# Kernel optimization log

Hardware: AMD Instinct MI355X
Metric: run time of the kernel (lower is better)

## Reference

```python
import jax, jax.numpy as jnp
import numpy as np

N_NODES = 100000
E_HALF = 2000000  # edges come in two mirrored halves (two classes per node pair)
IN_DIM, HID = 5, 16


def setup_inputs() -> dict:
    key = jax.random.key(0)
    ks = jax.random.split(key, 8)
    x = jax.random.normal(ks[0], (N_NODES, IN_DIM), dtype=jnp.float32)
    e_half = jax.random.randint(ks[1], (2, E_HALF), 0, N_NODES)
    edges = jnp.concatenate([e_half, e_half], axis=1)  # [2, 2*E_HALF]
    edge_attr = jax.random.uniform(ks[2], (2 * E_HALF, 2), dtype=jnp.float32)
    detector_labels = jax.random.bernoulli(ks[3], 0.5, (N_NODES,))
    s = 1.0 / np.sqrt(IN_DIM)
    W_rel = jax.random.uniform(ks[4], (HID, IN_DIM), minval=-s, maxval=s, dtype=jnp.float32)
    b_rel = jax.random.uniform(ks[5], (HID,), minval=-s, maxval=s, dtype=jnp.float32)
    W_root = jax.random.uniform(ks[6], (HID, IN_DIM), minval=-s, maxval=s, dtype=jnp.float32)
    s2 = 1.0 / np.sqrt(2 * HID + 1)
    k7, k8 = jax.random.split(ks[7])
    W_lin = jax.random.uniform(k7, (1, 2 * HID + 1), minval=-s2, maxval=s2, dtype=jnp.float32)
    b_lin = jax.random.uniform(k8, (1,), minval=-s2, maxval=s2, dtype=jnp.float32)
    return {
        "x": x, "edges": edges, "edge_attr": edge_attr,
        "detector_labels": detector_labels,
        "W_rel": W_rel, "b_rel": b_rel, "W_root": W_root,
        "W_lin": W_lin, "b_lin": b_lin,
    }


def reference(x, edges, edge_attr, detector_labels, W_rel, b_rel, W_root, W_lin, b_lin):
    N = x.shape[0]
    src, dst = edges[0], edges[1]
    # GraphConv(aggr='add'): out_i = W_root x_i + W_rel * sum_{(j->i)} w_e * x_j + b_rel
    w = edge_attr[:, 1]
    msg = x[src] * w[:, None]                                  # [E, 5]
    agg = jax.ops.segment_sum(msg, dst, num_segments=N)        # [N, 5]
    h = jnp.tanh(agg @ W_rel.T + b_rel + x @ W_root.T)         # [N, 16]
    # SplitSyndromes: keep edges whose both endpoints are detector nodes
    valid = detector_labels[src] & detector_labels[dst]
    vidx = jnp.nonzero(valid)[0]                               # data-dependent (eager)
    e = edges[:, vidx]
    ea = edge_attr[vidx]
    # gather-concat-linear edge scoring
    feat = jnp.concatenate([h[e[0]], ea[:, :1], h[e[1]]], axis=-1)  # [nv, 33]
    score = feat @ W_lin.T + b_lin                             # [nv, 1]
    nv = score.shape[0]
    half = nv // 2
    score2 = score.reshape(-1, half)                           # [2, half]
    classes2 = ea[:, 1].reshape(-1, half)
    mi = jnp.argmin(score2, axis=0)
    cols = jnp.arange(half)
    return e[:, :half], score2[mi, cols], classes2[mi, cols]
```

## Files before the change

kernel.cpp:

```cpp
#include <hip/hip_runtime.h>
#include <hip/hip_bf16.h>

#define HID 16
#define IN_DIM 5
#define PAD 8

#define FXS 64.0f
#define FXI 0.015625f

__global__ void pack_labels(const int* __restrict__ lab, unsigned long long* __restrict__ bits,
                            int N) {
    int n = blockIdx.x * 256 + threadIdx.x;
    bool p = (n < N) && (lab[n] != 0);
    unsigned long long m = __ballot(p);
    if ((threadIdx.x & 63) == 0) bits[n >> 6] = m;
}

__global__ void scatter_count(const int* __restrict__ src, const int* __restrict__ dst,
                              const unsigned long long* __restrict__ bits,
                              const float2* __restrict__ ea2,
                              const float* __restrict__ x,
                              const float* __restrict__ Wlin,
                              unsigned long long* __restrict__ agg,
                              int* __restrict__ counts,
                              int* __restrict__ stS, int* __restrict__ stD,
                              float* __restrict__ stP, float* __restrict__ stC,
                              int EH) {
    int i = blockIdx.x * 256 + threadIdx.x;
    bool v = false;
    int s = 0, d = 0;
    float scpart = 0.f, cls = 0.f;
    if (i < EH) {
        s = src[i];
        d = dst[i];
        bool ls = (bits[s >> 6] >> (s & 63)) & 1;
        bool ld = (bits[d >> 6] >> (d & 63)) & 1;
        v = ls && ld;
        if (ld || v) {
            float2 eaA = ea2[i];
            float2 eaB = ea2[(size_t)i + EH];
            if (ld) {
                float w = eaA.y + eaB.y;
                const float* xs = x + (size_t)s * IN_DIM;
                unsigned long long a = 0;
#pragma unroll
                for (int k = 0; k < IN_DIM; k++) {
                    int q = __float2int_rn(xs[k] * w * FXS);
                    a += (unsigned long long)(long long)q << (12 * k);
                }
                atomicAdd(&agg[(size_t)d * PAD], a);
            }
            if (v) {
                float w16 = Wlin[HID];
                float p0 = w16 * eaA.x;
                float p1 = w16 * eaB.x;
                if (p1 < p0) { scpart = p1; cls = eaB.y; }
                else         { scpart = p0; cls = eaA.y; }
            }
        }
    }
    unsigned long long m = __ballot(v);
    int lane = threadIdx.x & 63, wid = threadIdx.x >> 6;
    __shared__ int wc[4];
    if (lane == 0) wc[wid] = __popcll(m);
    __syncthreads();
    if (threadIdx.x == 0) counts[blockIdx.x] = wc[0] + wc[1] + wc[2] + wc[3];
    if (!v) return;
    int wexcl = 0;
    for (int k = 0; k < wid; k++) wexcl += wc[k];
    int slot = blockIdx.x * 256 + wexcl + __popcll(m & ((1ull << lane) - 1ull));
    stS[slot] = s;
    stD[slot] = d;
    stP[slot] = scpart;
    stC[slot] = cls;
}

__device__ __forceinline__ float decode_field(unsigned long long& T) {
    int r = (int)(T & 0xFFFull);
    int s = (r >= 2048) ? r - 4096 : r;
    T = (T - (unsigned long long)(long long)s) >> 12;
    return (float)s * FXI;
}

__global__ void compute_uv(const float* __restrict__ x,
                           const unsigned long long* __restrict__ agg,
                           const int* __restrict__ lab,
                           const float* __restrict__ Wrel, const float* __restrict__ brel,
                           const float* __restrict__ Wroot, const float* __restrict__ Wlin,
                           float2* __restrict__ uv, int N) {
    __shared__ float sWrel[HID * IN_DIM];
    __shared__ float sWroot[HID * IN_DIM];
    __shared__ float sBrel[HID];
    __shared__ float sWl[2 * HID + 1];
    int t = threadIdx.x;
    if (t < HID * IN_DIM) sWrel[t] = Wrel[t];
    else if (t < 2 * HID * IN_DIM) sWroot[t - HID * IN_DIM] = Wroot[t - HID * IN_DIM];
    else if (t < 2 * HID * IN_DIM + HID) sBrel[t - 2 * HID * IN_DIM] = brel[t - 2 * HID * IN_DIM];
    else if (t < 2 * HID * IN_DIM + HID + 2 * HID + 1)
        sWl[t - 2 * HID * IN_DIM - HID] = Wlin[t - 2 * HID * IN_DIM - HID];
    __syncthreads();

    int n = blockIdx.x * 256 + threadIdx.x;
    if (n >= N) return;
    if (!lab[n]) return;

    unsigned long long T = agg[(size_t)n * PAD];
    float a[IN_DIM], xv[IN_DIM];
#pragma unroll
    for (int d = 0; d < IN_DIM; d++) a[d] = decode_field(T);
#pragma unroll
    for (int d = 0; d < IN_DIM; d++) xv[d] = x[(size_t)n * IN_DIM + d];

    float u = 0.f, vv = 0.f;
#pragma unroll
    for (int k = 0; k < HID; k++) {
        float acc = sBrel[k];
#pragma unroll
        for (int d = 0; d < IN_DIM; d++)
            acc += a[d] * sWrel[k * IN_DIM + d] + xv[d] * sWroot[k * IN_DIM + d];
        float hk = tanhf(acc);
        u += sWl[k] * hk;
        vv += sWl[HID + 1 + k] * hk;
    }
    uv[n] = make_float2(u, vv);
}

__global__ void scan_counts(const int* __restrict__ counts, int* __restrict__ offs, int nb) {
    __shared__ int waveSums[16];
    int tid = threadIdx.x;
    int base = tid * 8;
    int vals[8];
    int tsum = 0;
#pragma unroll
    for (int k = 0; k < 8; k++) {
        int idx = base + k;
        vals[k] = (idx < nb) ? counts[idx] : 0;
        tsum += vals[k];
    }
    int lane = tid & 63, wid = tid >> 6;
    int scan = tsum;
#pragma unroll
    for (int off = 1; off < 64; off <<= 1) {
        int u = __shfl_up(scan, off, 64);
        if (lane >= off) scan += u;
    }
    if (lane == 63) waveSums[wid] = scan;
    __syncthreads();
    if (wid == 0 && lane < 16) {
        int s = waveSums[lane];
#pragma unroll
        for (int off = 1; off < 16; off <<= 1) {
            int u = __shfl_up(s, off, 64);
            if (lane >= off) s += u;
        }
        waveSums[lane] = s;
    }
    __syncthreads();
    int waveBase = (wid > 0) ? waveSums[wid - 1] : 0;
    int excl = waveBase + scan - tsum;
#pragma unroll
    for (int k = 0; k < 8; k++) {
        int idx = base + k;
        if (idx < nb) offs[idx] = excl;
        excl += vals[k];
    }
}

__global__ void emit_out(const int* __restrict__ stS, const int* __restrict__ stD,
                         const float* __restrict__ stP, const float* __restrict__ stC,
                         const float2* __restrict__ uv, const float* __restrict__ blin,
                         const int* __restrict__ counts, const int* __restrict__ offs,
                         float* __restrict__ out, int K) {
    int b = blockIdx.x;
    int cnt = counts[b];
    int t = threadIdx.x;
    if (t >= cnt) return;
    int slot = b * 256 + t;
    int s = stS[slot];
    int d = stD[slot];
    float sc = blin[0] + uv[s].x + uv[d].y + stP[slot];
    int r = offs[b] + t;
    out[r] = (float)s;
    out[(size_t)K + r] = (float)d;
    out[2 * (size_t)K + r] = sc;
    out[3 * (size_t)K + r] = stC[slot];
}

extern "C" void kernel_launch(void* const* d_in, const int* in_sizes, int n_in,
                              void* d_out, int out_size, void* d_ws, size_t ws_size,
                              hipStream_t stream) {
    const float* x     = (const float*)d_in[0];
    const int*   edges = (const int*)d_in[1];
    const float* ea    = (const float*)d_in[2];
    const int*   lab   = (const int*)d_in[3];
    const float* Wrel  = (const float*)d_in[4];
    const float* brel  = (const float*)d_in[5];
    const float* Wroot = (const float*)d_in[6];
    const float* Wlin  = (const float*)d_in[7];
    const float* blin  = (const float*)d_in[8];

    const int N  = in_sizes[0] / IN_DIM;
    const int E  = in_sizes[1] / 2;
    const int EH = E / 2;
    const int K  = out_size / 4;

    const int* src = edges;
    const int* dst = edges + E;
    const float2* ea2 = (const float2*)ea;
    const int nb = (EH + 255) / 256;
    const int nslots = nb * 256;

    char* ws = (char*)d_ws;
    size_t off = 0;
    unsigned long long* agg = (unsigned long long*)(ws + off); off += (size_t)N * PAD * 8;
    float2* uv = (float2*)(ws + off); off += (size_t)N * 8;
    unsigned long long* bits = (unsigned long long*)(ws + off);
    off += (size_t)(((N + 63) / 64) * 8 + 255) / 256 * 256;
    int* counts = (int*)(ws + off); off += (size_t)(nb * 4 + 255) / 256 * 256;
    int* offs   = (int*)(ws + off); off += (size_t)(nb * 4 + 255) / 256 * 256;
    int*   stS = (int*)(ws + off);   off += (size_t)nslots * 4;
    int*   stD = (int*)(ws + off);   off += (size_t)nslots * 4;
    float* stP = (float*)(ws + off); off += (size_t)nslots * 4;
    float* stC = (float*)(ws + off); off += (size_t)nslots * 4;

    float* out = (float*)d_out;

    hipMemsetAsync(agg, 0, (size_t)N * PAD * 8, stream);
    pack_labels<<<(N + 255) / 256, 256, 0, stream>>>(lab, bits, N);
    scatter_count<<<nb, 256, 0, stream>>>(src, dst, bits, ea2, x, Wlin, agg, counts,
                                          stS, stD, stP, stC, EH);
    compute_uv<<<(N + 255) / 256, 256, 0, stream>>>(x, agg, lab, Wrel, brel, Wroot, Wlin, uv, N);
    scan_counts<<<1, 1024, 0, stream>>>(counts, offs, nb);
    emit_out<<<nb, 256, 0, stream>>>(stS, stD, stP, stC, uv, blin, counts, offs, out, K);
}
```

Measured before the change: 181.1 us.

## Process four edges per thread with vector loads and padded x, packed staging

The scatter kernel now handles four edges per thread with int4/float4 loads of src, dst and edge attributes. A padded 8-float copy of x is built in pack_labels so gathers become two float4 loads. Staging is packed into one float4 array, and emit_out loops over up to 1024 slots per block. The intent is fewer memory transactions and more loads in flight, at the cost of an extra padded-x buffer, a wave-level shuffle scan, and loads issued even for edges whose destination is not a detector node.

```diff
diff --git a/kernel.cpp b/kernel.cpp
--- a/kernel.cpp
+++ b/kernel.cpp
@@ -1,78 +1,154 @@
 #include <hip/hip_runtime.h>
-#include <hip/hip_bf16.h>
 
 #define HID 16
 #define IN_DIM 5
 #define PAD 8
+#define EPT 4
 
 #define FXS 64.0f
 #define FXI 0.015625f
 
-__global__ void pack_labels(const int* __restrict__ lab, unsigned long long* __restrict__ bits,
+__global__ void pack_labels(const int* __restrict__ lab, const float* __restrict__ x,
+                            unsigned long long* __restrict__ bits, float* __restrict__ xp,
                             int N) {
     int n = blockIdx.x * 256 + threadIdx.x;
     bool p = (n < N) && (lab[n] != 0);
     unsigned long long m = __ballot(p);
-    if ((threadIdx.x & 63) == 0) bits[n >> 6] = m;
-}
-
-__global__ void scatter_count(const int* __restrict__ src, const int* __restrict__ dst,
-                              const unsigned long long* __restrict__ bits,
-                              const float2* __restrict__ ea2,
-                              const float* __restrict__ x,
-                              const float* __restrict__ Wlin,
-                              unsigned long long* __restrict__ agg,
-                              int* __restrict__ counts,
-                              int* __restrict__ stS, int* __restrict__ stD,
-                              float* __restrict__ stP, float* __restrict__ stC,
-                              int EH) {
-    int i = blockIdx.x * 256 + threadIdx.x;
-    bool v = false;
-    int s = 0, d = 0;
-    float scpart = 0.f, cls = 0.f;
-    if (i < EH) {
-        s = src[i];
-        d = dst[i];
-        bool ls = (bits[s >> 6] >> (s & 63)) & 1;
-        bool ld = (bits[d >> 6] >> (d & 63)) & 1;
-        v = ls && ld;
-        if (ld || v) {
-            float2 eaA = ea2[i];
-            float2 eaB = ea2[(size_t)i + EH];
-            if (ld) {
-                float w = eaA.y + eaB.y;
-                const float* xs = x + (size_t)s * IN_DIM;
-                unsigned long long a = 0;
-#pragma unroll
-                for (int k = 0; k < IN_DIM; k++) {
-                    int q = __float2int_rn(xs[k] * w * FXS);
-                    a += (unsigned long long)(long long)q << (12 * k);
-                }
-                atomicAdd(&agg[(size_t)d * PAD], a);
-            }
-            if (v) {
-                float w16 = Wlin[HID];
-                float p0 = w16 * eaA.x;
-                float p1 = w16 * eaB.x;
-                if (p1 < p0) { scpart = p1; cls = eaB.y; }
-                else         { scpart = p0; cls = eaA.y; }
-            }
+    if (((threadIdx.x & 63) == 0) && n < N) bits[n >> 6] = m;
+    if (n < N) {
+        float4 a;
+        a.x = x[(size_t)n * IN_DIM + 0];
+        a.y = x[(size_t)n * IN_DIM + 1];
+        a.z = x[(size_t)n * IN_DIM + 2];
+        a.w = x[(size_t)n * IN_DIM + 3];
+        *(float4*)(xp + (size_t)n * 8) = a;
+        float4 b;
+        b.x = x[(size_t)n * IN_DIM + 4];
+        b.y = 0.f; b.z = 0.f; b.w = 0.f;
+        *(float4*)(xp + (size_t)n * 8 + 4) = b;
+    }
+}
+
+__global__ __launch_bounds__(256, 4) void scatter_count(
+        const int* __restrict__ src, const int* __restrict__ dst,
+        const unsigned long long* __restrict__ bits,
+        const float2* __restrict__ ea2,
+        const float* __restrict__ xp,
+        const float* __restrict__ Wlin,
+        unsigned long long* __restrict__ agg,
+        int* __restrict__ counts,
+        float4* __restrict__ st4,
+        int EH) {
+    const int tid = threadIdx.x;
+    const int i0 = (blockIdx.x * 256 + tid) * EPT;
+
+    int s[EPT], d[EPT];
+    float2 eaA[EPT], eaB[EPT];
+    bool act[EPT];
+
+    if (i0 + EPT <= EH && ((EH & 1) == 0)) {
+        int4 s4 = *(const int4*)(src + i0);
+        int4 d4 = *(const int4*)(dst + i0);
+        s[0] = s4.x; s[1] = s4.y; s[2] = s4.z; s[3] = s4.w;
+        d[0] = d4.x; d[1] = d4.y; d[2] = d4.z; d[3] = d4.w;
+        float4 a0 = *(const float4*)(ea2 + i0);
+        float4 a1 = *(const float4*)(ea2 + i0 + 2);
+        float4 b0 = *(const float4*)(ea2 + (size_t)i0 + EH);
+        float4 b1 = *(const float4*)(ea2 + (size_t)i0 + EH + 2);
+        eaA[0] = make_float2(a0.x, a0.y); eaA[1] = make_float2(a0.z, a0.w);
+        eaA[2] = make_float2(a1.x, a1.y); eaA[3] = make_float2(a1.z, a1.w);
+        eaB[0] = make_float2(b0.x, b0.y); eaB[1] = make_float2(b0.z, b0.w);
+        eaB[2] = make_float2(b1.x, b1.y); eaB[3] = make_float2(b1.z, b1.w);
+#pragma unroll
+        for (int k = 0; k < EPT; k++) act[k] = true;
+    } else {
+#pragma unroll
+        for (int k = 0; k < EPT; k++) {
+            int i = i0 + k;
+            act[k] = (i < EH);
+            s[k] = act[k] ? src[i] : 0;
+            d[k] = act[k] ? dst[i] : 0;
+            eaA[k] = act[k] ? ea2[i] : make_float2(0.f, 0.f);
+            eaB[k] = act[k] ? ea2[(size_t)i + EH] : make_float2(0.f, 0.f);
         }
     }
-    unsigned long long m = __ballot(v);
-    int lane = threadIdx.x & 63, wid = threadIdx.x >> 6;
+
+    bool ld[EPT], vl[EPT];
+#pragma unroll
+    for (int k = 0; k < EPT; k++) {
+        bool ls = (bits[s[k] >> 6] >> (s[k] & 63)) & 1;
+        bool lv = (bits[d[k] >> 6] >> (d[k] & 63)) & 1;
+        ld[k] = act[k] && lv;
+        vl[k] = ld[k] && ls;
+    }
+
+    float4 xa[EPT], xb[EPT];
+#pragma unroll
+    for (int k = 0; k < EPT; k++) {
+        const float* xs = xp + (size_t)s[k] * 8;
+        xa[k] = *(const float4*)xs;
+        xb[k] = *(const float4*)(xs + 4);
+    }
+
+#pragma unroll
+    for (int k = 0; k < EPT; k++) {
+        if (ld[k]) {
+            float w = (eaA[k].y + eaB[k].y) * FXS;
+            unsigned long long a = 0;
+            int q0 = __float2int_rn(xa[k].x * w);
+            int q1 = __float2int_rn(xa[k].y * w);
+            int q2 = __float2int_rn(xa[k].z * w);
+            int q3 = __float2int_rn(xa[k].w * w);
+            int q4 = __float2int_rn(xb[k].x * w);
+            a += (unsigned long long)(long long)q0;
+            a += (unsigned long long)(long long)q1 << 12;
+            a += (unsigned long long)(long long)q2 << 24;
+            a += (unsigned long long)(long long)q3 << 36;
+            a += (unsigned long long)(long long)q4 << 48;
+            atomicAdd(&agg[(size_t)d[k] * PAD], a);
+        }
+    }
+
+    float w16 = Wlin[HID];
+    float scpart[EPT], cls[EPT];
+#pragma unroll
+    for (int k = 0; k < EPT; k++) {
+        float p0 = w16 * eaA[k].x;
+        float p1 = w16 * eaB[k].x;
+        if (p1 < p0) { scpart[k] = p1; cls[k] = eaB[k].y; }
+        else         { scpart[k] = p0; cls[k] = eaA[k].y; }
+    }
+
+    unsigned m4 = 0;
+#pragma unroll
+    for (int k = 0; k < EPT; k++) m4 |= (vl[k] ? (1u << k) : 0u);
+    int cnt = __popc(m4);
+    int lane = tid & 63, wid = tid >> 6;
+    int scan = cnt;
+#pragma unroll
+    for (int off = 1; off < 64; off <<= 1) {
+        int u = __shfl_up(scan, off, 64);
+        if (lane >= off) scan += u;
+    }
     __shared__ int wc[4];
-    if (lane == 0) wc[wid] = __popcll(m);
+    if (lane == 63) wc[wid] = scan;
     __syncthreads();
-    if (threadIdx.x == 0) counts[blockIdx.x] = wc[0] + wc[1] + wc[2] + wc[3];
-    if (!v) return;
+    if (tid == 0) counts[blockIdx.x] = wc[0] + wc[1] + wc[2] + wc[3];
     int wexcl = 0;
-    for (int k = 0; k < wid; k++) wexcl += wc[k];
-    int slot = blockIdx.x * 256 + wexcl + __popcll(m & ((1ull << lane) - 1ull));
-    stS[slot] = s;
-    stD[slot] = d;
-    stP[slot] = scpart;
-    stC[slot] = cls;
+#pragma unroll
+    for (int k = 0; k < 4; k++) if (k < wid) wexcl += wc[k];
+    int idx = blockIdx.x * (256 * EPT) + wexcl + (scan - cnt);
+#pragma unroll
+    for (int k = 0; k < EPT; k++) {
+        if (vl[k]) {
+            float4 r;
+            r.x = __int_as_float(s[k]);
+            r.y = __int_as_float(d[k]);
+            r.z = scpart[k];
+            r.w = cls[k];
+            st4[idx++] = r;
+        }
+    }
 }
 
 __device__ __forceinline__ float decode_field(unsigned long long& T) {
@@ -82,7 +158,7 @@
     return (float)s * FXI;
 }
 
-__global__ void compute_uv(const float* __restrict__ x,
+__global__ void compute_uv(const float* __restrict__ xp,
                            const unsigned long long* __restrict__ agg,
                            const int* __restrict__ lab,
                            const float* __restrict__ Wrel, const float* __restrict__ brel,
@@ -108,8 +184,9 @@
     float a[IN_DIM], xv[IN_DIM];
 #pragma unroll
     for (int d = 0; d < IN_DIM; d++) a[d] = decode_field(T);
-#pragma unroll
-    for (int d = 0; d < IN_DIM; d++) xv[d] = x[(size_t)n * IN_DIM + d];
+    float4 x0 = *(const float4*)(xp + (size_t)n * 8);
+    xv[0] = x0.x; xv[1] = x0.y; xv[2] = x0.z; xv[3] = x0.w;
+    xv[4] = xp[(size_t)n * 8 + 4];
 
     float u = 0.f, vv = 0.f;
 #pragma unroll
@@ -166,24 +243,25 @@
     }
 }
 
-__global__ void emit_out(const int* __restrict__ stS, const int* __restrict__ stD,
-                         const float* __restrict__ stP, const float* __restrict__ stC,
-                         const float2* __restrict__ uv, const float* __restrict__ blin,
+__global__ void emit_out(const float4* __restrict__ st4,
+                         const float* __restrict__ uvf, const float* __restrict__ blin,
                          const int* __restrict__ counts, const int* __restrict__ offs,
                          float* __restrict__ out, int K) {
     int b = blockIdx.x;
     int cnt = counts[b];
-    int t = threadIdx.x;
-    if (t >= cnt) return;
-    int slot = b * 256 + t;
-    int s = stS[slot];
-    int d = stD[slot];
-    float sc = blin[0] + uv[s].x + uv[d].y + stP[slot];
-    int r = offs[b] + t;
-    out[r] = (float)s;
-    out[(size_t)K + r] = (float)d;
-    out[2 * (size_t)K + r] = sc;
-    out[3 * (size_t)K + r] = stC[slot];
+    int base = offs[b];
+    float bl = blin[0];
+    for (int t = threadIdx.x; t < cnt; t += 256) {
+        float4 r = st4[(size_t)b * (256 * EPT) + t];
+        int s = __float_as_int(r.x);
+        int d = __float_as_int(r.y);
+        float sc = bl + uvf[2 * (size_t)s] + uvf[2 * (size_t)d + 1] + r.z;
+        int ro = base + t;
+        out[ro] = (float)s;
+        out[(size_t)K + ro] = (float)d;
+        out[2 * (size_t)K + ro] = sc;
+        out[3 * (size_t)K + ro] = r.w;
+    }
 }
 
 extern "C" void kernel_launch(void* const* d_in, const int* in_sizes, int n_in,
@@ -207,8 +285,9 @@
     const int* src = edges;
     const int* dst = edges + E;
     const float2* ea2 = (const float2*)ea;
-    const int nb = (EH + 255) / 256;
-    const int nslots = nb * 256;
+    const int EPB = 256 * EPT;
+    const int nb = (EH + EPB - 1) / EPB;
+    const int nslots = nb * EPB;
 
     char* ws = (char*)d_ws;
     size_t off = 0;
@@ -216,20 +295,18 @@
     float2* uv = (float2*)(ws + off); off += (size_t)N * 8;
     unsigned long long* bits = (unsigned long long*)(ws + off);
     off += (size_t)(((N + 63) / 64) * 8 + 255) / 256 * 256;
+    float* xp = (float*)(ws + off); off += (size_t)N * 8 * 4;
     int* counts = (int*)(ws + off); off += (size_t)(nb * 4 + 255) / 256 * 256;
     int* offs   = (int*)(ws + off); off += (size_t)(nb * 4 + 255) / 256 * 256;
-    int*   stS = (int*)(ws + off);   off += (size_t)nslots * 4;
-    int*   stD = (int*)(ws + off);   off += (size_t)nslots * 4;
-    float* stP = (float*)(ws + off); off += (size_t)nslots * 4;
-    float* stC = (float*)(ws + off); off += (size_t)nslots * 4;
+    float4* st4 = (float4*)(ws + off); off += (size_t)nslots * 16;
 
     float* out = (float*)d_out;
 
     hipMemsetAsync(agg, 0, (size_t)N * PAD * 8, stream);
-    pack_labels<<<(N + 255) / 256, 256, 0, stream>>>(lab, bits, N);
-    scatter_count<<<nb, 256, 0, stream>>>(src, dst, bits, ea2, x, Wlin, agg, counts,
-                                          stS, stD, stP, stC, EH);
-    compute_uv<<<(N + 255) / 256, 256, 0, stream>>>(x, agg, lab, Wrel, brel, Wroot, Wlin, uv, N);
+    pack_labels<<<(N + 255) / 256, 256, 0, stream>>>(lab, x, bits, xp, N);
+    scatter_count<<<nb, 256, 0, stream>>>(src, dst, bits, ea2, xp, Wlin, agg, counts,
+                                          st4, EH);
+    compute_uv<<<(N + 255) / 256, 256, 0, stream>>>(xp, agg, lab, Wrel, brel, Wroot, Wlin, uv, N);
     scan_counts<<<1, 1024, 0, stream>>>(counts, offs, nb);
-    emit_out<<<nb, 256, 0, stream>>>(stS, stD, stP, stC, uv, blin, counts, offs, out, K);
-}
+    emit_out<<<nb, 256, 0, stream>>>(st4, (const float*)uv, blin, counts, offs, out, K);
+}
```

Result: no change. 178.3 us (-1.5%).
